# Kernel tuning notes

Hardware: AMD Instinct MI355X
Metric: run time of the kernel (lower is better)

## Reference

```python
import jax, jax.numpy as jnp
import numpy as np

LN_EPS = 1e-5


def setup_inputs() -> dict:
    key = jax.random.key(0)
    ks = jax.random.split(key, 10)
    b, n, m, d, e = 2, 4096, 32, 128, 64
    return {
        "t_ij": jax.random.normal(ks[0], (b, n, m, d), dtype=jnp.float32),
        "x1": jax.random.normal(ks[1], (b, n, d, 3), dtype=jnp.float32),
        "x2": jax.random.normal(ks[2], (b, n, d, 5), dtype=jnp.float32),
        "neighbor_indices": jax.random.randint(ks[3], (b, n, m), 0, n),
        "to_queries": jax.random.normal(ks[4], (d, e), dtype=jnp.float32),
        "to_keys1": jax.random.normal(ks[5], (d, e), dtype=jnp.float32),
        "to_keys2": jax.random.normal(ks[6], (d, e), dtype=jnp.float32),
        "ln_weight": jnp.ones((2 * e,), dtype=jnp.float32),
        "edge_w": jax.random.normal(ks[7], (2 * e, d), dtype=jnp.float32) / np.sqrt(2 * e),
        "res_w": jax.random.normal(ks[8], (d, d), dtype=jnp.float32) / np.sqrt(d),
    }


def _degree_inner_product(xl, to_queries, to_keys, neighbor_indices):
    # xl: [b n d ml]; projections over channel dim d -> e
    q = jnp.einsum('bndm,de->bnem', xl, to_queries)   # [b n e ml]
    k = jnp.einsum('bndm,de->bnem', xl, to_keys)      # [b n e ml]
    # gather neighbor keys: [b n j e ml]
    kg = jax.vmap(lambda kk, idx: kk[idx])(k, neighbor_indices)
    # inner product over multiplicity ml, per feature e: [b n j e]
    return jnp.einsum('bnem,bnjem->bnje', q, kg)


def reference(t_ij, x1, x2, neighbor_indices, to_queries, to_keys1, to_keys2,
              ln_weight, edge_w, res_w):
    ip1 = _degree_inner_product(x1, to_queries, to_keys1, neighbor_indices)
    ip2 = _degree_inner_product(x2, to_queries, to_keys2, neighbor_indices)
    w_ij = jnp.concatenate([ip1, ip2], axis=-1)  # [b n j 2e]
    # LayerNorm over last dim, weight only (bias=False)
    mu = jnp.mean(w_ij, axis=-1, keepdims=True)
    var = jnp.mean((w_ij - mu) ** 2, axis=-1, keepdims=True)
    w_ij = (w_ij - mu) * jax.lax.rsqrt(var + LN_EPS) * ln_weight
    edge_out = jax.nn.sigmoid(jnp.einsum('bnje,ed->bnjd', w_ij, edge_w))
    res_out = jnp.einsum('bnjd,de->bnje', t_ij, res_w)
    return edge_out + res_out
```

## Files before the change

kernel.cpp:

```cpp
#include <hip/hip_runtime.h>

#define B_ 2
#define N_ 4096
#define M_ 32
#define D_ 128
#define E_ 64
#define LN_EPS 1e-5f
#define WST 136
#define TOT (B_ * N_)
#define FGRID 1536

typedef __bf16 bf16x8 __attribute__((ext_vector_type(8)));
typedef float  f32x4  __attribute__((ext_vector_type(4)));

__global__ __launch_bounds__(256) void proj_kernel(
    const float* __restrict__ x1, const float* __restrict__ x2,
    const float* __restrict__ Wq, const float* __restrict__ Wk1,
    const float* __restrict__ Wk2,
    float* __restrict__ qws, __bf16* __restrict__ kws)
{
    __shared__ float xs[4][D_ * 8];
    const int lane = threadIdx.x & 63;
    const int wv   = threadIdx.x >> 6;
    const int bn   = blockIdx.x * 4 + wv;
    float* xw = xs[wv];
    const float* __restrict__ x1p = x1 + (size_t)bn * (D_ * 3);
    const float* __restrict__ x2p = x2 + (size_t)bn * (D_ * 5);
    for (int i = lane; i < D_ * 3; i += 64) xw[(i / 3) * 8 + (i % 3)]     = x1p[i];
    for (int i = lane; i < D_ * 5; i += 64) xw[(i / 5) * 8 + 3 + (i % 5)] = x2p[i];
    __syncthreads();

    float q[8] = {0.f,0.f,0.f,0.f,0.f,0.f,0.f,0.f};
    float k[8] = {0.f,0.f,0.f,0.f,0.f,0.f,0.f,0.f};
    #pragma unroll 4
    for (int d = 0; d < D_; ++d) {
        const float4 xa = *(const float4*)&xw[d * 8];
        const float4 xb = *(const float4*)&xw[d * 8 + 4];
        const float wq  = Wq [d * E_ + lane];
        const float wk1 = Wk1[d * E_ + lane];
        const float wk2 = Wk2[d * E_ + lane];
        q[0] += xa.x * wq;  q[1] += xa.y * wq;  q[2] += xa.z * wq;  q[3] += xa.w * wq;
        q[4] += xb.x * wq;  q[5] += xb.y * wq;  q[6] += xb.z * wq;  q[7] += xb.w * wq;
        k[0] += xa.x * wk1; k[1] += xa.y * wk1; k[2] += xa.z * wk1;
        k[3] += xa.w * wk2; k[4] += xb.x * wk2; k[5] += xb.y * wk2;
        k[6] += xb.z * wk2; k[7] += xb.w * wk2;
    }
    float4* qo = (float4*)(qws + ((size_t)bn * E_ + lane) * 8);
    qo[0] = make_float4(q[0], q[1], q[2], q[3]);
    qo[1] = make_float4(q[4], q[5], q[6], q[7]);
    bf16x8 kb;
    #pragma unroll
    for (int s = 0; s < 8; ++s) kb[s] = (__bf16)k[s];
    *(bf16x8*)(kws + ((size_t)bn * E_ + lane) * 8) = kb;
}

__global__ __launch_bounds__(256, 3) void fused_kernel(
    const float* __restrict__ t_ij, const int* __restrict__ nidx,
    const float* __restrict__ qws, const __bf16* __restrict__ kws,
    const float* __restrict__ ln_w,
    const float* __restrict__ edge_w, const float* __restrict__ res_w,
    float* __restrict__ out)
{
    __shared__ __bf16 wbuf[3][M_ * WST];

    const int t    = threadIdx.x;
    const int lane = t & 63;
    const int wvu  = t >> 6;
    const int r16  = lane & 15;
    const int quad = lane >> 4;
    const int n0   = wvu * 32;

    bf16x8 bE[2][4], bR[2][4];
    #pragma unroll
    for (int nt = 0; nt < 2; ++nt) {
        const int col = n0 + nt * 16 + r16;
        #pragma unroll
        for (int ks = 0; ks < 4; ++ks) {
            const int k0 = ks * 32 + quad * 8;
            bf16x8 fe, fr;
            #pragma unroll
            for (int j = 0; j < 8; ++j) {
                fe[j] = (__bf16)edge_w[(k0 + j) * D_ + col];
                fr[j] = (__bf16)res_w [(k0 + j) * D_ + col];
            }
            bE[nt][ks] = fe;
            bR[nt][ks] = fr;
        }
    }

    const float lnlo = ln_w[lane];
    const float lnhi = ln_w[64 + lane];

    auto phaseW = [&](int bn, __bf16* buf) {
        const int    b  = bn >> 12;
        const size_t jb = (size_t)bn * M_;
        const float* qp = qws + ((size_t)bn * E_ + lane) * 8;
        const float4 qa = *(const float4*)qp;
        const float4 qb = *(const float4*)(qp + 4);
        #pragma unroll 4
        for (int jj = 0; jj < 8; ++jj) {
            const int j  = wvu * 8 + jj;
            const int nj = nidx[jb + j];
            const bf16x8 kv =
                *(const bf16x8*)&kws[((size_t)(b * N_ + nj) * E_ + lane) * 8];
            const float wlo = qa.x * (float)kv[0] + qa.y * (float)kv[1]
                            + qa.z * (float)kv[2];
            const float whi = qa.w * (float)kv[3] + qb.x * (float)kv[4]
                            + qb.y * (float)kv[5] + qb.z * (float)kv[6]
                            + qb.w * (float)kv[7];
            float s1 = wlo + whi;
            float s2 = wlo * wlo + whi * whi;
            #pragma unroll
            for (int off = 1; off < 64; off <<= 1) {
                s1 += __shfl_xor(s1, off, 64);
                s2 += __shfl_xor(s2, off, 64);
            }
            const float mu  = s1 * (1.f / 128.f);
            const float var = fmaxf(s2 * (1.f / 128.f) - mu * mu, 0.f);
            const float rs  = rsqrtf(var + LN_EPS);
            buf[j * WST + lane]      = (__bf16)((wlo - mu) * rs * lnlo);
            buf[j * WST + 64 + lane] = (__bf16)((whi - mu) * rs * lnhi);
        }
    };

    auto tload = [&](int bn, bf16x8* tf) {
        const float* tp = t_ij + ((size_t)bn * M_ + r16) * D_;
        #pragma unroll
        for (int ks = 0; ks < 4; ++ks) {
            const int ko = ks * 32 + quad * 8;
            const float4 t0 = *(const float4*)(tp + ko);
            const float4 t1 = *(const float4*)(tp + ko + 4);
            bf16x8 a;
            a[0]=(__bf16)t0.x; a[1]=(__bf16)t0.y; a[2]=(__bf16)t0.z; a[3]=(__bf16)t0.w;
            a[4]=(__bf16)t1.x; a[5]=(__bf16)t1.y; a[6]=(__bf16)t1.z; a[7]=(__bf16)t1.w;
            tf[ks] = a;
        }
    };

    auto phaseM = [&](int bn, const __bf16* buf, const bf16x8* tf) {
        const size_t jb = (size_t)bn * M_;
        bf16x8 aT1[4];
        {
            const float* tp = t_ij + (jb + 16 + r16) * D_;
            #pragma unroll
            for (int ks = 0; ks < 4; ++ks) {
                const int ko = ks * 32 + quad * 8;
                const float4 t0 = *(const float4*)(tp + ko);
                const float4 t1 = *(const float4*)(tp + ko + 4);
                bf16x8 a;
                a[0]=(__bf16)t0.x; a[1]=(__bf16)t0.y; a[2]=(__bf16)t0.z; a[3]=(__bf16)t0.w;
                a[4]=(__bf16)t1.x; a[5]=(__bf16)t1.y; a[6]=(__bf16)t1.z; a[7]=(__bf16)t1.w;
                aT1[ks] = a;
            }
        }
        f32x4 accE[2][2], accR[2][2];
        #pragma unroll
        for (int mt = 0; mt < 2; ++mt)
            #pragma unroll
            for (int nt = 0; nt < 2; ++nt) {
                accE[mt][nt] = (f32x4){0.f,0.f,0.f,0.f};
                accR[mt][nt] = (f32x4){0.f,0.f,0.f,0.f};
            }
        #pragma unroll
        for (int ks = 0; ks < 4; ++ks) {
            const bf16x8 aW0 = *(const bf16x8*)&buf[r16 * WST + ks * 32 + quad * 8];
            const bf16x8 aW1 = *(const bf16x8*)&buf[(16 + r16) * WST + ks * 32 + quad * 8];
            #pragma unroll
            for (int nt = 0; nt < 2; ++nt) {
                accE[0][nt] = __builtin_amdgcn_mfma_f32_16x16x32_bf16(aW0,    bE[nt][ks], accE[0][nt], 0, 0, 0);
                accR[0][nt] = __builtin_amdgcn_mfma_f32_16x16x32_bf16(tf[ks], bR[nt][ks], accR[0][nt], 0, 0, 0);
                accE[1][nt] = __builtin_amdgcn_mfma_f32_16x16x32_bf16(aW1,    bE[nt][ks], accE[1][nt], 0, 0, 0);
                accR[1][nt] = __builtin_amdgcn_mfma_f32_16x16x32_bf16(aT1[ks],bR[nt][ks], accR[1][nt], 0, 0, 0);
            }
        }
        #pragma unroll
        for (int mt = 0; mt < 2; ++mt)
            #pragma unroll
            for (int nt = 0; nt < 2; ++nt)
                #pragma unroll
                for (int rr = 0; rr < 4; ++rr) {
                    const int row = mt * 16 + quad * 4 + rr;
                    const int col = n0 + nt * 16 + r16;
                    const float e  = accE[mt][nt][rr];
                    const float sg = 1.f / (1.f + __expf(-e));
                    out[(jb + row) * D_ + col] = sg + accR[mt][nt][rr];
                }
    };

    const int stride = gridDim.x;
    int bn = blockIdx.x;
    bf16x8 tf[4];
    phaseW(bn, wbuf[0]);
    tload(bn, tf);
    int buf = 0;
    for (; bn < TOT; bn += stride) {
        const int nb   = bn + stride;
        const int nbuf = (buf == 2) ? 0 : buf + 1;
        if (nb < TOT) phaseW(nb, wbuf[nbuf]);
        __syncthreads();
        phaseM(bn, wbuf[buf], tf);
        if (nb < TOT) tload(nb, tf);
        buf = nbuf;
    }
}

extern "C" void kernel_launch(void* const* d_in, const int* in_sizes, int n_in,
                              void* d_out, int out_size, void* d_ws, size_t ws_size,
                              hipStream_t stream) {
    const float* t_ij = (const float*)d_in[0];
    const float* x1   = (const float*)d_in[1];
    const float* x2   = (const float*)d_in[2];
    const int*   nidx = (const int*)  d_in[3];
    const float* Wq   = (const float*)d_in[4];
    const float* Wk1  = (const float*)d_in[5];
    const float* Wk2  = (const float*)d_in[6];
    const float* lnw  = (const float*)d_in[7];
    const float* eww  = (const float*)d_in[8];
    const float* rww  = (const float*)d_in[9];
    float* out = (float*)d_out;

    float*  qws = (float*)d_ws;
    __bf16* kws = (__bf16*)(qws + (size_t)TOT * E_ * 8);

    proj_kernel<<<TOT / 4, 256, 0, stream>>>(x1, x2, Wq, Wk1, Wk2, qws, kws);
    fused_kernel<<<FGRID, 256, 0, stream>>>(t_ij, nidx, qws, kws, lnw, eww, rww, out);
}
```

Measured before the change: 394.3 us.

## Swap MFMA operands for float4 stores, DPP wave reductions, fast rcp, halve grid

Swaps the A/B operands of the MFMA calls so each lane's accumulator holds four consecutive output columns. The epilogue can then write a single float4 per tile instead of four scattered scalar stores. The layer-norm reductions move from a shuffle-xor loop to DPP and ds_swizzle steps, the sigmoid uses a hardware reciprocal, and the persistent grid is halved. These cut store transactions and reduction latency, but the smaller grid may reduce latency hiding and the approximate reciprocal slightly changes numerics.

```diff
diff --git a/kernel.cpp b/kernel.cpp
--- a/kernel.cpp
+++ b/kernel.cpp
@@ -8,7 +8,7 @@
 #define LN_EPS 1e-5f
 #define WST 136
 #define TOT (B_ * N_)
-#define FGRID 1536
+#define FGRID 768
 
 typedef __bf16 bf16x8 __attribute__((ext_vector_type(8)));
 typedef float  f32x4  __attribute__((ext_vector_type(4)));
@@ -54,6 +54,20 @@
     *(bf16x8*)(kws + ((size_t)bn * E_ + lane) * 8) = kb;
 }
 
+__device__ __forceinline__ float dpp_red16(float v) {
+    v += __int_as_float(__builtin_amdgcn_update_dpp(0, __float_as_int(v), 0xB1,  0xF, 0xF, true));
+    v += __int_as_float(__builtin_amdgcn_update_dpp(0, __float_as_int(v), 0x4E,  0xF, 0xF, true));
+    v += __int_as_float(__builtin_amdgcn_update_dpp(0, __float_as_int(v), 0x141, 0xF, 0xF, true));
+    v += __int_as_float(__builtin_amdgcn_update_dpp(0, __float_as_int(v), 0x140, 0xF, 0xF, true));
+    return v;
+}
+__device__ __forceinline__ float wave_sum(float v) {
+    v = dpp_red16(v);
+    v += __int_as_float(__builtin_amdgcn_ds_swizzle(__float_as_int(v), 0x401F));
+    v += __shfl_xor(v, 32, 64);
+    return v;
+}
+
 __global__ __launch_bounds__(256, 3) void fused_kernel(
     const float* __restrict__ t_ij, const int* __restrict__ nidx,
     const float* __restrict__ qws, const __bf16* __restrict__ kws,
@@ -108,13 +122,8 @@
             const float whi = qa.w * (float)kv[3] + qb.x * (float)kv[4]
                             + qb.y * (float)kv[5] + qb.z * (float)kv[6]
                             + qb.w * (float)kv[7];
-            float s1 = wlo + whi;
-            float s2 = wlo * wlo + whi * whi;
-            #pragma unroll
-            for (int off = 1; off < 64; off <<= 1) {
-                s1 += __shfl_xor(s1, off, 64);
-                s2 += __shfl_xor(s2, off, 64);
-            }
+            const float s1 = wave_sum(wlo + whi);
+            const float s2 = wave_sum(wlo * wlo + whi * whi);
             const float mu  = s1 * (1.f / 128.f);
             const float var = fmaxf(s2 * (1.f / 128.f) - mu * mu, 0.f);
             const float rs  = rsqrtf(var + LN_EPS);
@@ -167,24 +176,25 @@
             const bf16x8 aW1 = *(const bf16x8*)&buf[(16 + r16) * WST + ks * 32 + quad * 8];
             #pragma unroll
             for (int nt = 0; nt < 2; ++nt) {
-                accE[0][nt] = __builtin_amdgcn_mfma_f32_16x16x32_bf16(aW0,    bE[nt][ks], accE[0][nt], 0, 0, 0);
-                accR[0][nt] = __builtin_amdgcn_mfma_f32_16x16x32_bf16(tf[ks], bR[nt][ks], accR[0][nt], 0, 0, 0);
-                accE[1][nt] = __builtin_amdgcn_mfma_f32_16x16x32_bf16(aW1,    bE[nt][ks], accE[1][nt], 0, 0, 0);
-                accR[1][nt] = __builtin_amdgcn_mfma_f32_16x16x32_bf16(aT1[ks],bR[nt][ks], accR[1][nt], 0, 0, 0);
+                accE[0][nt] = __builtin_amdgcn_mfma_f32_16x16x32_bf16(bE[nt][ks], aW0,     accE[0][nt], 0, 0, 0);
+                accR[0][nt] = __builtin_amdgcn_mfma_f32_16x16x32_bf16(bR[nt][ks], tf[ks],  accR[0][nt], 0, 0, 0);
+                accE[1][nt] = __builtin_amdgcn_mfma_f32_16x16x32_bf16(bE[nt][ks], aW1,     accE[1][nt], 0, 0, 0);
+                accR[1][nt] = __builtin_amdgcn_mfma_f32_16x16x32_bf16(bR[nt][ks], aT1[ks], accR[1][nt], 0, 0, 0);
             }
         }
         #pragma unroll
         for (int mt = 0; mt < 2; ++mt)
             #pragma unroll
-            for (int nt = 0; nt < 2; ++nt)
+            for (int nt = 0; nt < 2; ++nt) {
+                float4 o;
                 #pragma unroll
                 for (int rr = 0; rr < 4; ++rr) {
-                    const int row = mt * 16 + quad * 4 + rr;
-                    const int col = n0 + nt * 16 + r16;
                     const float e  = accE[mt][nt][rr];
-                    const float sg = 1.f / (1.f + __expf(-e));
-                    out[(jb + row) * D_ + col] = sg + accR[mt][nt][rr];
+                    const float sg = __builtin_amdgcn_rcpf(1.f + __expf(-e));
+                    (&o.x)[rr] = sg + accR[mt][nt][rr];
                 }
+                *(float4*)(out + (jb + mt * 16 + r16) * D_ + n0 + nt * 16 + quad * 4) = o;
+            }
     };
 
     const int stride = gridDim.x;
```

After: 370.3 us. 6.1% less time.
